# Performance work log

Measured on AMD Instinct MI355X. Metric: run time of the kernel, lower is better.

## Reference

```python
import jax, jax.numpy as jnp
import numpy as np

# Config (matches init_kwargs)
B, H, N, K, M = 64, 2, 512, 64, 16  # batch, num_of_hom, max_num_of_points, K, man_dim
EPS = 1e-7
MAX_NORM = 1.0 - 1e-5  # clip radius strictly inside the Poincare ball


def _norm(x):
    return jnp.sqrt(jnp.sum(x * x, axis=-1, keepdims=True))


def _exp0(v):
    # Poincare exp map at origin (c=1): tanh(||v||) * v / ||v||
    n = jnp.maximum(_norm(v), EPS)
    return jnp.tanh(n) * v / n


def _log0(y):
    # Poincare log map at origin (c=1): arctanh(||y||) * y / ||y||, norm clipped inside ball
    n = jnp.maximum(_norm(y), EPS)
    return jnp.arctanh(jnp.minimum(n, MAX_NORM)) * y / n


def _process_dgm(dgm, theta_h):
    # dgm: (B, N, 2)  theta_h: (K, M)
    b = dgm.shape[0]
    td = jnp.tile(dgm, (1, K, 1))                        # (B, K*N, 2) -- K blocks of N points
    td = jnp.pad(td, ((0, 0), (0, 0), (0, M - 2)))       # (B, K*N, M)
    tt = jnp.tile(theta_h, (1, N)).reshape(-1, M)        # (K*N, M) -- theta_k repeated N times
    x = _exp0(td) + tt                                   # parametrization + learned offset
    tangent_x = _log0(x)                                 # log map to tangent space at origin
    tangent_x = tangent_x.reshape(b, N, K, M)            # mirrors TF reshape exactly (row-major)
    sums = jnp.sum(tangent_x, axis=1)                    # (B, K, M)
    x_dgm = _exp0(sums)                                  # exp map back to manifold
    y_dgm = _log0(x_dgm)                                 # chart coordinates
    return y_dgm.reshape(-1, K, M)


def setup_inputs() -> dict:
    key = jax.random.key(0)
    k1, k2 = jax.random.split(key)
    inputs = jax.random.uniform(k1, (B, H, N, 2), dtype=jnp.float32)   # (birth, death) pairs
    theta = jax.random.uniform(k2, (H, K, M), dtype=jnp.float32) * 0.05  # tf.random_uniform_initializer
    return {"inputs": inputs, "theta": theta}


def reference(inputs, theta):
    out_0 = _process_dgm(inputs[:, 0, :, :], theta[0])[:, None, :, :]  # (B,1,K,M)
    out_1 = _process_dgm(inputs[:, 1, :, :], theta[1])[:, None, :, :]  # (B,1,K,M)
    return jnp.concatenate([out_0, out_1], axis=1)                      # (B,2,K,M)
```

## Files before the change

### kernel.cpp

```cpp
#include <hip/hip_runtime.h>

constexpr int Bsz = 64;
constexpr int Hn  = 2;
constexpr int Np  = 512;
constexpr int Kk  = 64;
constexpr int Mm  = 16;

constexpr int TS = 68;

#define EPSf      1e-7f
#define MAXN      (1.0f - 1e-5f)
#define ATANH_MAX 6.1030338f
#define HALF_LN2  0.34657359f

__global__ __launch_bounds__(256) void PManifold_kernel(
    const float* __restrict__ inp,
    const float* __restrict__ theta,
    float* __restrict__ out)
{
    __shared__ __align__(16) float sTcol[Mm * TS];
    __shared__ __align__(16) float sRed[4][3 * TS];

    const int tid  = threadIdx.x;
    const int lane = tid & 63;
    const int wav  = tid >> 6;
    const int g    = blockIdx.x * 4 + wav;
    const int kp   = g & 63;
    const int bh   = g >> 6;
    const int h    = bh & (Hn - 1);

    {
        const int r  = tid >> 2;
        const int cb = (tid & 3) << 2;
        const float4 q = *reinterpret_cast<const float4*>(theta + (size_t)(h * Kk + r) * Mm + cb);
        sTcol[(cb + 0) * TS + r] = (cb == 0) ? 1.0f : q.x;
        sTcol[(cb + 1) * TS + r] = (cb == 0) ? 1.0f : q.y;
        sTcol[(cb + 2) * TS + r] = q.z;
        sTcol[(cb + 3) * TS + r] = q.w;
    }
    __syncthreads();

    float t0, t1, c;
    {
        const float4* tq = reinterpret_cast<const float4*>(theta) + (size_t)(h * Kk + lane) * 4;
        float4 q0 = tq[0], q1 = tq[1], q2 = tq[2], q3 = tq[3];
        t0 = q0.x; t1 = q0.y;
        c  = q0.z * q0.z + q0.w * q0.w;
        c  = fmaf(q1.x, q1.x, fmaf(q1.y, q1.y, fmaf(q1.z, q1.z, fmaf(q1.w, q1.w, c))));
        c  = fmaf(q2.x, q2.x, fmaf(q2.y, q2.y, fmaf(q2.z, q2.z, fmaf(q2.w, q2.w, c))));
        c  = fmaf(q3.x, q3.x, fmaf(q3.y, q3.y, fmaf(q3.z, q3.z, fmaf(q3.w, q3.w, c))));
    }

    float E0, E1;
    {
        const int p = lane & 7;
        const float2* ip = reinterpret_cast<const float2*>(inp) + (size_t)bh * Np;
        float2 dd = ip[(p << 6) + kp];
        float nd = sqrtf(fmaf(dd.x, dd.x, dd.y * dd.y));
        float nc = fmaxf(nd, EPSf);
        float ex = __expf(2.0f * nc);
        float sc = (ex - 1.0f) * __frcp_rn((ex + 1.0f) * nc);
        E0 = sc * dd.x;
        E1 = sc * dd.y;
    }
    float e0[8], e1[8];
    #pragma unroll
    for (int p = 0; p < 8; ++p) {
        e0[p] = __int_as_float(__builtin_amdgcn_readlane(__float_as_int(E0), p));
        e1[p] = __int_as_float(__builtin_amdgcn_readlane(__float_as_int(E1), p));
    }

    float At = 0.0f, S0 = 0.0f, S1 = 0.0f;
    #pragma unroll
    for (int p = 0; p < 8; ++p) {
        float x0 = e0[p] + t0;
        float x1 = e1[p] + t1;
        float u  = fmaf(x0, x0, fmaf(x1, x1, c));
        u        = fmaxf(u, 1e-14f);
        float rs = rsqrtf(u);
        float rc = fminf(u * rs, MAXN);
        float Q  = (1.0f + rc) * __frcp_rn(1.0f - rc);
        float tt = __log2f(Q) * rs;
        float a  = HALF_LN2 * tt;
        At += tt;
        S0 = fmaf(a, x0, S0);
        S1 = fmaf(a, x1, S1);
    }
    const float A = HALF_LN2 * At;

    sRed[wav][lane]          = S0;
    sRed[wav][TS + lane]     = S1;
    sRed[wav][2 * TS + lane] = A;
    __syncthreads();

    const int m = lane & 15;
    const int q = lane >> 4;
    const float* valArr = &sRed[wav][(m < 2) ? m * TS : 2 * TS];
    const float* muCol  = &sTcol[m * TS];
    float acc = 0.0f;
    #pragma unroll
    for (int jj = 0; jj < 4; ++jj) {
        float4 v4 = *reinterpret_cast<const float4*>(valArr + (q << 4) + (jj << 2));
        float4 u4 = *reinterpret_cast<const float4*>(muCol  + (q << 4) + (jj << 2));
        acc = fmaf(v4.x, u4.x, fmaf(v4.y, u4.y, fmaf(v4.z, u4.z, fmaf(v4.w, u4.w, acc))));
    }
    acc += __shfl_xor(acc, 16, 64);
    acc += __shfl_xor(acc, 32, 64);

    float w = acc * acc;
    #pragma unroll
    for (int off = 1; off < 16; off <<= 1) w += __shfl_xor(w, off, 64);
    float nn  = fmaxf(sqrtf(w), EPSf);
    float gsc = (nn < ATANH_MAX) ? 1.0f : __fdividef(ATANH_MAX, nn);

    if (lane < 16) {
        out[(size_t)g * Mm + m] = gsc * acc;
    }
}

extern "C" void kernel_launch(void* const* d_in, const int* in_sizes, int n_in,
                              void* d_out, int out_size, void* d_ws, size_t ws_size,
                              hipStream_t stream) {
    const float* inp   = (const float*)d_in[0];
    const float* theta = (const float*)d_in[1];
    float*       out   = (float*)d_out;

    const int total_waves = Bsz * Hn * Kk;
    dim3 grid(total_waves / 4), block(256);
    hipLaunchKernelGGL(PManifold_kernel, grid, block, 0, stream, inp, theta, out);
}
```

Measured before the change: 61.05 us.

## Compute two output rows per wavefront and use raw hardware reciprocal

Each wavefront now produces two output rows (kp and kp+32), handling 16 points per lane instead of 8 and launching half as many waves. Per-wave fixed costs such as the theta load, the shared-memory staging, the syncs and the shuffle reductions are amortised over twice the work. The correctly rounded reciprocal is also replaced by the raw hardware rcp intrinsic. The trade-off is fewer waves in flight (2048 instead of 4096) and more registers per lane, plus a small loss of reciprocal accuracy.

```diff
diff --git a/kernel.cpp b/kernel.cpp
--- a/kernel.cpp
+++ b/kernel.cpp
@@ -13,20 +13,22 @@
 #define ATANH_MAX 6.1030338f
 #define HALF_LN2  0.34657359f
 
+__device__ __forceinline__ float fast_rcp(float x) { return __builtin_amdgcn_rcpf(x); }
+
 __global__ __launch_bounds__(256) void PManifold_kernel(
     const float* __restrict__ inp,
     const float* __restrict__ theta,
     float* __restrict__ out)
 {
     __shared__ __align__(16) float sTcol[Mm * TS];
-    __shared__ __align__(16) float sRed[4][3 * TS];
+    __shared__ __align__(16) float sRed[4][6 * TS];
 
     const int tid  = threadIdx.x;
     const int lane = tid & 63;
     const int wav  = tid >> 6;
     const int g    = blockIdx.x * 4 + wav;
-    const int kp   = g & 63;
-    const int bh   = g >> 6;
+    const int kp   = g & 31;
+    const int bh   = g >> 5;
     const int h    = bh & (Hn - 1);
 
     {
@@ -53,68 +55,86 @@
 
     float E0, E1;
     {
-        const int p = lane & 7;
+        const int pp  = lane & 15;
+        const int idx = ((pp & 7) << 6) + kp + ((pp >> 3) << 5);
         const float2* ip = reinterpret_cast<const float2*>(inp) + (size_t)bh * Np;
-        float2 dd = ip[(p << 6) + kp];
+        float2 dd = ip[idx];
         float nd = sqrtf(fmaf(dd.x, dd.x, dd.y * dd.y));
         float nc = fmaxf(nd, EPSf);
         float ex = __expf(2.0f * nc);
-        float sc = (ex - 1.0f) * __frcp_rn((ex + 1.0f) * nc);
+        float sc = (ex - 1.0f) * fast_rcp((ex + 1.0f) * nc);
         E0 = sc * dd.x;
         E1 = sc * dd.y;
     }
-    float e0[8], e1[8];
+    float e0[16], e1[16];
     #pragma unroll
-    for (int p = 0; p < 8; ++p) {
+    for (int p = 0; p < 16; ++p) {
         e0[p] = __int_as_float(__builtin_amdgcn_readlane(__float_as_int(E0), p));
         e1[p] = __int_as_float(__builtin_amdgcn_readlane(__float_as_int(E1), p));
     }
 
-    float At = 0.0f, S0 = 0.0f, S1 = 0.0f;
+    float Aa = 0.0f, S0a = 0.0f, S1a = 0.0f;
+    float Ab = 0.0f, S0b = 0.0f, S1b = 0.0f;
     #pragma unroll
-    for (int p = 0; p < 8; ++p) {
+    for (int p = 0; p < 16; ++p) {
         float x0 = e0[p] + t0;
         float x1 = e1[p] + t1;
         float u  = fmaf(x0, x0, fmaf(x1, x1, c));
         u        = fmaxf(u, 1e-14f);
         float rs = rsqrtf(u);
         float rc = fminf(u * rs, MAXN);
-        float Q  = (1.0f + rc) * __frcp_rn(1.0f - rc);
+        float Q  = (1.0f + rc) * fast_rcp(1.0f - rc);
         float tt = __log2f(Q) * rs;
         float a  = HALF_LN2 * tt;
-        At += tt;
-        S0 = fmaf(a, x0, S0);
-        S1 = fmaf(a, x1, S1);
+        if (p < 8) { Aa += tt; S0a = fmaf(a, x0, S0a); S1a = fmaf(a, x1, S1a); }
+        else       { Ab += tt; S0b = fmaf(a, x0, S0b); S1b = fmaf(a, x1, S1b); }
     }
-    const float A = HALF_LN2 * At;
 
-    sRed[wav][lane]          = S0;
-    sRed[wav][TS + lane]     = S1;
-    sRed[wav][2 * TS + lane] = A;
+    sRed[wav][0 * TS + lane] = S0a;
+    sRed[wav][1 * TS + lane] = S1a;
+    sRed[wav][2 * TS + lane] = HALF_LN2 * Aa;
+    sRed[wav][3 * TS + lane] = S0b;
+    sRed[wav][4 * TS + lane] = S1b;
+    sRed[wav][5 * TS + lane] = HALF_LN2 * Ab;
     __syncthreads();
 
     const int m = lane & 15;
     const int q = lane >> 4;
-    const float* valArr = &sRed[wav][(m < 2) ? m * TS : 2 * TS];
-    const float* muCol  = &sTcol[m * TS];
-    float acc = 0.0f;
+    const int voff = (m < 2) ? m * TS : 2 * TS;
+    const float* valA  = &sRed[wav][voff];
+    const float* valB  = &sRed[wav][3 * TS + voff];
+    const float* muCol = &sTcol[m * TS];
+    float accA = 0.0f, accB = 0.0f;
     #pragma unroll
     for (int jj = 0; jj < 4; ++jj) {
-        float4 v4 = *reinterpret_cast<const float4*>(valArr + (q << 4) + (jj << 2));
-        float4 u4 = *reinterpret_cast<const float4*>(muCol  + (q << 4) + (jj << 2));
-        acc = fmaf(v4.x, u4.x, fmaf(v4.y, u4.y, fmaf(v4.z, u4.z, fmaf(v4.w, u4.w, acc))));
+        const int o = (q << 4) + (jj << 2);
+        float4 u4 = *reinterpret_cast<const float4*>(muCol + o);
+        float4 va = *reinterpret_cast<const float4*>(valA + o);
+        float4 vb = *reinterpret_cast<const float4*>(valB + o);
+        accA = fmaf(va.x, u4.x, fmaf(va.y, u4.y, fmaf(va.z, u4.z, fmaf(va.w, u4.w, accA))));
+        accB = fmaf(vb.x, u4.x, fmaf(vb.y, u4.y, fmaf(vb.z, u4.z, fmaf(vb.w, u4.w, accB))));
     }
-    acc += __shfl_xor(acc, 16, 64);
-    acc += __shfl_xor(acc, 32, 64);
+    accA += __shfl_xor(accA, 16, 64);
+    accA += __shfl_xor(accA, 32, 64);
+    accB += __shfl_xor(accB, 16, 64);
+    accB += __shfl_xor(accB, 32, 64);
 
-    float w = acc * acc;
+    float wA = accA * accA, wB = accB * accB;
     #pragma unroll
-    for (int off = 1; off < 16; off <<= 1) w += __shfl_xor(w, off, 64);
-    float nn  = fmaxf(sqrtf(w), EPSf);
-    float gsc = (nn < ATANH_MAX) ? 1.0f : __fdividef(ATANH_MAX, nn);
+    for (int off = 1; off < 16; off <<= 1) {
+        wA += __shfl_xor(wA, off, 64);
+        wB += __shfl_xor(wB, off, 64);
+    }
+    float nnA  = fmaxf(sqrtf(wA), EPSf);
+    float nnB  = fmaxf(sqrtf(wB), EPSf);
+    float gA = (nnA < ATANH_MAX) ? 1.0f : __fdividef(ATANH_MAX, nnA);
+    float gB = (nnB < ATANH_MAX) ? 1.0f : __fdividef(ATANH_MAX, nnB);
 
-    if (lane < 16) {
-        out[(size_t)g * Mm + m] = gsc * acc;
+    if (lane < 32) {
+        const int    which = lane >> 4;
+        const size_t row   = (size_t)(bh * Kk + kp + (which << 5));
+        const float  val   = which ? (gB * accB) : (gA * accA);
+        out[row * Mm + m] = val;
     }
 }
 
@@ -125,7 +145,7 @@
     const float* theta = (const float*)d_in[1];
     float*       out   = (float*)d_out;
 
-    const int total_waves = Bsz * Hn * Kk;
+    const int total_waves = Bsz * Hn * Kk / 2;
     dim3 grid(total_waves / 4), block(256);
     hipLaunchKernelGGL(PManifold_kernel, grid, block, 0, stream, inp, theta, out);
 }
```

Result: faster. 59.52 us (median of 2 runs) (-2.5%).

## Process four output rows per wavefront and use fast hardware reciprocal

Applied to the files above, without the earlier changes.

Each wavefront now handles four k-groups instead of one. It computes 32 exp-mapped points per wave, where it used to compute 8 per group, and keeps four sets of partial sums. The grid shrinks fourfold, which cuts per-wave setup overhead such as the theta loads, shared-memory staging and block syncs. It also swaps the correctly rounded __frcp_rn for the hardware rcp builtin, trading some precision in the tanh and atanh terms. Register pressure rises with the 32-entry arrays, and there are fewer blocks to fill the GPU.

```diff
diff --git a/kernel.cpp b/kernel.cpp
--- a/kernel.cpp
+++ b/kernel.cpp
@@ -13,20 +13,22 @@
 #define ATANH_MAX 6.1030338f
 #define HALF_LN2  0.34657359f
 
+__device__ __forceinline__ float fast_rcp(float x) { return __builtin_amdgcn_rcpf(x); }
+
 __global__ __launch_bounds__(256) void PManifold_kernel(
     const float* __restrict__ inp,
     const float* __restrict__ theta,
     float* __restrict__ out)
 {
     __shared__ __align__(16) float sTcol[Mm * TS];
-    __shared__ __align__(16) float sRed[4][3 * TS];
+    __shared__ __align__(16) float sRed[4][12 * TS];
 
     const int tid  = threadIdx.x;
     const int lane = tid & 63;
     const int wav  = tid >> 6;
     const int g    = blockIdx.x * 4 + wav;
-    const int kp   = g & 63;
-    const int bh   = g >> 6;
+    const int kp   = g & 15;
+    const int bh   = g >> 4;
     const int h    = bh & (Hn - 1);
 
     {
@@ -53,69 +55,89 @@
 
     float E0, E1;
     {
-        const int p = lane & 7;
+        const int pp  = lane & 31;
+        const int idx = ((pp & 7) << 6) + kp + ((pp >> 3) << 4);
         const float2* ip = reinterpret_cast<const float2*>(inp) + (size_t)bh * Np;
-        float2 dd = ip[(p << 6) + kp];
+        float2 dd = ip[idx];
         float nd = sqrtf(fmaf(dd.x, dd.x, dd.y * dd.y));
         float nc = fmaxf(nd, EPSf);
         float ex = __expf(2.0f * nc);
-        float sc = (ex - 1.0f) * __frcp_rn((ex + 1.0f) * nc);
+        float sc = (ex - 1.0f) * fast_rcp((ex + 1.0f) * nc);
         E0 = sc * dd.x;
         E1 = sc * dd.y;
     }
-    float e0[8], e1[8];
+    float e0[32], e1[32];
     #pragma unroll
-    for (int p = 0; p < 8; ++p) {
+    for (int p = 0; p < 32; ++p) {
         e0[p] = __int_as_float(__builtin_amdgcn_readlane(__float_as_int(E0), p));
         e1[p] = __int_as_float(__builtin_amdgcn_readlane(__float_as_int(E1), p));
     }
 
-    float At = 0.0f, S0 = 0.0f, S1 = 0.0f;
+    float Aj[4]  = {0.0f, 0.0f, 0.0f, 0.0f};
+    float S0j[4] = {0.0f, 0.0f, 0.0f, 0.0f};
+    float S1j[4] = {0.0f, 0.0f, 0.0f, 0.0f};
     #pragma unroll
-    for (int p = 0; p < 8; ++p) {
+    for (int p = 0; p < 32; ++p) {
+        const int j = p >> 3;
         float x0 = e0[p] + t0;
         float x1 = e1[p] + t1;
         float u  = fmaf(x0, x0, fmaf(x1, x1, c));
         u        = fmaxf(u, 1e-14f);
         float rs = rsqrtf(u);
         float rc = fminf(u * rs, MAXN);
-        float Q  = (1.0f + rc) * __frcp_rn(1.0f - rc);
+        float Q  = (1.0f + rc) * fast_rcp(1.0f - rc);
         float tt = __log2f(Q) * rs;
         float a  = HALF_LN2 * tt;
-        At += tt;
-        S0 = fmaf(a, x0, S0);
-        S1 = fmaf(a, x1, S1);
+        Aj[j] += tt;
+        S0j[j] = fmaf(a, x0, S0j[j]);
+        S1j[j] = fmaf(a, x1, S1j[j]);
     }
-    const float A = HALF_LN2 * At;
 
-    sRed[wav][lane]          = S0;
-    sRed[wav][TS + lane]     = S1;
-    sRed[wav][2 * TS + lane] = A;
+    #pragma unroll
+    for (int j = 0; j < 4; ++j) {
+        sRed[wav][(3 * j + 0) * TS + lane] = S0j[j];
+        sRed[wav][(3 * j + 1) * TS + lane] = S1j[j];
+        sRed[wav][(3 * j + 2) * TS + lane] = HALF_LN2 * Aj[j];
+    }
     __syncthreads();
 
     const int m = lane & 15;
     const int q = lane >> 4;
-    const float* valArr = &sRed[wav][(m < 2) ? m * TS : 2 * TS];
-    const float* muCol  = &sTcol[m * TS];
-    float acc = 0.0f;
+    const int voff = (m < 2) ? m * TS : 2 * TS;
+    const float* muCol = &sTcol[m * TS];
+    float acc[4] = {0.0f, 0.0f, 0.0f, 0.0f};
     #pragma unroll
     for (int jj = 0; jj < 4; ++jj) {
-        float4 v4 = *reinterpret_cast<const float4*>(valArr + (q << 4) + (jj << 2));
-        float4 u4 = *reinterpret_cast<const float4*>(muCol  + (q << 4) + (jj << 2));
-        acc = fmaf(v4.x, u4.x, fmaf(v4.y, u4.y, fmaf(v4.z, u4.z, fmaf(v4.w, u4.w, acc))));
+        const int o = (q << 4) + (jj << 2);
+        float4 u4 = *reinterpret_cast<const float4*>(muCol + o);
+        #pragma unroll
+        for (int j = 0; j < 4; ++j) {
+            float4 v4 = *reinterpret_cast<const float4*>(&sRed[wav][3 * j * TS + voff] + o);
+            acc[j] = fmaf(v4.x, u4.x, fmaf(v4.y, u4.y, fmaf(v4.z, u4.z, fmaf(v4.w, u4.w, acc[j]))));
+        }
     }
-    acc += __shfl_xor(acc, 16, 64);
-    acc += __shfl_xor(acc, 32, 64);
+    #pragma unroll
+    for (int j = 0; j < 4; ++j) {
+        acc[j] += __shfl_xor(acc[j], 16, 64);
+        acc[j] += __shfl_xor(acc[j], 32, 64);
+    }
 
-    float w = acc * acc;
+    float gsc[4];
     #pragma unroll
-    for (int off = 1; off < 16; off <<= 1) w += __shfl_xor(w, off, 64);
-    float nn  = fmaxf(sqrtf(w), EPSf);
-    float gsc = (nn < ATANH_MAX) ? 1.0f : __fdividef(ATANH_MAX, nn);
+    for (int j = 0; j < 4; ++j) {
+        float w = acc[j] * acc[j];
+        #pragma unroll
+        for (int off = 1; off < 16; off <<= 1) w += __shfl_xor(w, off, 64);
+        float nn = fmaxf(sqrtf(w), EPSf);
+        gsc[j] = (nn < ATANH_MAX) ? 1.0f : __fdividef(ATANH_MAX, nn);
+    }
 
-    if (lane < 16) {
-        out[(size_t)g * Mm + m] = gsc * acc;
-    }
+    const int   which = lane >> 4;
+    float       val;
+    val = (which == 0) ? gsc[0] * acc[0] : ((which == 1) ? gsc[1] * acc[1]
+        : ((which == 2) ? gsc[2] * acc[2] : gsc[3] * acc[3]));
+    const size_t row = (size_t)(bh * Kk + kp + (which << 4));
+    out[row * Mm + m] = val;
 }
 
 extern "C" void kernel_launch(void* const* d_in, const int* in_sizes, int n_in,
@@ -125,7 +147,7 @@
     const float* theta = (const float*)d_in[1];
     float*       out   = (float*)d_out;
 
-    const int total_waves = Bsz * Hn * Kk;
+    const int total_waves = Bsz * Hn * Kk / 4;
     dim3 grid(total_waves / 4), block(256);
     hipLaunchKernelGGL(PManifold_kernel, grid, block, 0, stream, inp, theta, out);
 }
```

Measured after the change: 59.88 us. No clear change (-1.9%).
